# Kernel optimization log

Hardware: AMD Instinct MI355X
Metric: run time of the kernel (lower is better)

The kernel has to match this reference:

```python
import jax, jax.numpy as jnp
import numpy as np

B, T, F, U = 32, 2048, 512, 512


def hard_sigmoid(x):
    # Keras hard_sigmoid: clip(0.2*x + 0.5, 0, 1)
    return jnp.clip(0.2 * x + 0.5, 0.0, 1.0)


def setup_inputs() -> dict:
    key = jax.random.key(0)
    ks = jax.random.split(key, 10)
    s = 0.05  # keep pre-activations in a sane range
    return {
        "x": jax.random.normal(ks[0], (B, F), jnp.float32),
        "h": jax.random.normal(ks[1], (B, U), jnp.float32),
        "annotations": jax.random.normal(ks[2], (B, T, F), jnp.float32),
        "kernel": jax.random.normal(ks[3], (F, 3 * U), jnp.float32) * s,
        "recurrent_kernel": jax.random.normal(ks[4], (U, 3 * U), jnp.float32) * s,
        "attention_kernel": jax.random.normal(ks[5], (F, 3 * U), jnp.float32) * s,
        "Wa": jax.random.normal(ks[6], (U, U), jnp.float32) * s,
        "Ua": jax.random.normal(ks[7], (F, U), jnp.float32) * s,
        "Va": jax.random.normal(ks[8], (U,), jnp.float32) * s,
        "bias": jnp.zeros((3 * U,), jnp.float32),
        "attention_bias": jnp.zeros((3 * U,), jnp.float32),
        "Wa_bias": jnp.zeros((U,), jnp.float32),
        "Ua_bias": jnp.zeros((U,), jnp.float32),
    }


def reference(x, h, annotations, kernel, recurrent_kernel, attention_kernel,
              Wa, Ua, Va, bias, attention_bias, Wa_bias, Ua_bias):
    u = h.shape[-1]
    # --- Bahdanau additive attention ---
    # pre: [B, T, U] = Wa h_{t-1} (broadcast over T) + Ua a_j
    pre = (h @ Wa + Wa_bias)[:, None, :] + annotations @ Ua + Ua_bias
    scores = jnp.einsum('btu,u->bt', jnp.tanh(pre), Va)          # [B, T]
    alpha = jax.nn.softmax(scores, axis=-1)                      # [B, T]
    c = jnp.einsum('bt,btf->bf', alpha, annotations)             # context [B, F]

    # --- GRU gates (reset_after=False, implementation 1 math, batched) ---
    xm = x @ kernel + bias                                       # [B, 3U]
    am = c @ attention_kernel + attention_bias                   # [B, 3U]
    x_z, x_r, x_h = xm[:, :u], xm[:, u:2 * u], xm[:, 2 * u:]
    a_z, a_r, a_h = am[:, :u], am[:, u:2 * u], am[:, 2 * u:]
    h_z = h @ recurrent_kernel[:, :u]
    h_r = h @ recurrent_kernel[:, u:2 * u]

    z = hard_sigmoid(x_z + h_z + a_z)                            # update gate
    r = hard_sigmoid(x_r + h_r + a_r)                            # reset gate
    hh = jnp.tanh(x_h + (r * h) @ recurrent_kernel[:, 2 * u:] + a_h)
    h_new = z * h + (1.0 - z) * hh
    return h_new
```

## Files before the change

kernel.cpp:

```cpp
#include <hip/hip_runtime.h>
#include <hip/hip_bf16.h>
#include <math.h>

#define BB 32
#define TT 2048
#define FF 512
#define UU 512

typedef __attribute__((ext_vector_type(4))) float f32x4;
typedef __attribute__((ext_vector_type(4))) short bf16x4;
typedef __attribute__((ext_vector_type(8))) short bf16x8;

__device__ inline short f2bf(float f) {
  union { __hip_bfloat16 h; short s; } u;
  u.h = __float2bfloat16(f);
  return u.s;
}

__device__ inline float bf2f(unsigned short s) {
  return __uint_as_float(((unsigned)s) << 16);
}

__device__ inline float tanh_fast(float x) {
  float e = __expf(2.0f * x);
  return 1.0f - 2.0f * __builtin_amdgcn_rcpf(e + 1.0f);
}


__global__ __launch_bounds__(256) void k01(
    const float* __restrict__ Ua, short* __restrict__ Up,
    const float* __restrict__ h, const float* __restrict__ Wa,
    const float* __restrict__ Wa_bias, const float* __restrict__ Ua_bias,
    float* __restrict__ hw) {
  const int bid = blockIdx.x;
  const int tid = threadIdx.x;
  if (bid < 128) {
    const int cell = bid * 4 + (tid >> 6);
    const int n16 = cell >> 4;
    const int k32 = cell & 15;
    const int l = tid & 63;
    const int n = n16 * 16 + (l & 15);
    const int g = l >> 4;
    bf16x8 v;
#pragma unroll
    for (int i = 0; i < 8; ++i) {
      int k = k32 * 32 + (i < 4 ? g * 4 + i : 16 + g * 4 + (i - 4));
      v[i] = f2bf(Ua[k * UU + n]);
    }
    *reinterpret_cast<bf16x8*>(Up + ((size_t)cell * 64 + l) * 8) = v;
  } else {
    int idx = (bid - 128) * 256 + tid;
    int b = idx >> 9;
    int u = idx & 511;
    float acc = Wa_bias[u] + Ua_bias[u];
    const float* hrow = h + b * UU;
#pragma unroll 8
    for (int f = 0; f < FF; ++f) acc += hrow[f] * Wa[f * UU + u];
    hw[idx] = acc;
  }
}

__global__ __launch_bounds__(512, 2) void k2_flash(
    const float* __restrict__ ann, const short* __restrict__ Up,
    const float* __restrict__ Va, const float* __restrict__ hw,
    float* __restrict__ mbuf, float* __restrict__ lbuf,
    float* __restrict__ cpart) {
  __shared__ short Af[65536];
  __shared__ float red[8][128];
  __shared__ float e_all[128];
  __shared__ float sred[128];
  __shared__ float wtmp[4];
  __shared__ float ctxp[8][512];
  const int tile = blockIdx.x;
  const int b = blockIdx.y;
  const int t0 = tile * 128;
  const int tid = threadIdx.x;
  const int w = tid >> 6;
  const int l = tid & 63;
  const int lo = l & 15;
  const int g = l >> 4;

  const float* annb = ann + ((size_t)b * TT + t0) * FF;
  const float* srow = annb + (size_t)(w * 16 + lo) * FF + g * 4;
  short* const afw = &Af[((w * 16) * 64 + l) * 8];

  const short* upb[4];
  upb[0] = Up + ((size_t)((w * 4 + 0) * 16) * 64 + l) * 8;
  upb[1] = Up + ((size_t)((w * 4 + 1) * 16) * 64 + l) * 8;
  upb[2] = Up + ((size_t)((w * 4 + 2) * 16) * 64 + l) * 8;
  upb[3] = Up + ((size_t)((w * 4 + 3) * 16) * 64 + l) * 8;

  f32x4 acc[8][4];
#pragma unroll
  for (int mf = 0; mf < 8; ++mf)
#pragma unroll
    for (int nf = 0; nf < 4; ++nf) acc[mf][nf] = (f32x4)0.f;

  f32x4 stg[2][2];
  bf16x8 bb[2][4];

  stg[0][0] = *reinterpret_cast<const f32x4*>(srow + 0 * 32);
  stg[0][1] = *reinterpret_cast<const f32x4*>(srow + 0 * 32 + 16);
  stg[1][0] = *reinterpret_cast<const f32x4*>(srow + 1 * 32);
  stg[1][1] = *reinterpret_cast<const f32x4*>(srow + 1 * 32 + 16);
#pragma unroll
  for (int nf = 0; nf < 4; ++nf) {
    bb[0][nf] = *reinterpret_cast<const bf16x8*>(upb[nf]);
    bb[1][nf] = *reinterpret_cast<const bf16x8*>(upb[nf] + 512);
  }
  {
    bf16x8 o;
    o[0] = f2bf(stg[0][0].x); o[1] = f2bf(stg[0][0].y);
    o[2] = f2bf(stg[0][0].z); o[3] = f2bf(stg[0][0].w);
    o[4] = f2bf(stg[0][1].x); o[5] = f2bf(stg[0][1].y);
    o[6] = f2bf(stg[0][1].z); o[7] = f2bf(stg[0][1].w);
    *reinterpret_cast<bf16x8*>(afw + 0 * 512) = o;
  }
  __syncthreads();

#pragma unroll
  for (int s = 0; s < 16; ++s) {
    if (s < 14) {
      stg[s & 1][0] = *reinterpret_cast<const f32x4*>(srow + (s + 2) * 32);
      stg[s & 1][1] = *reinterpret_cast<const f32x4*>(srow + (s + 2) * 32 + 16);
    }
    bf16x8 aA[8];
#pragma unroll
    for (int mf = 0; mf < 8; ++mf)
      aA[mf] = *reinterpret_cast<const bf16x8*>(
          &Af[((mf * 16 + s) * 64 + l) * 8]);
    __builtin_amdgcn_s_setprio(1);
#pragma unroll
    for (int mf = 0; mf < 8; ++mf)
#pragma unroll
      for (int nf = 0; nf < 4; ++nf)
        acc[mf][nf] = __builtin_amdgcn_mfma_f32_16x16x32_bf16(
            aA[mf], bb[s & 1][nf], acc[mf][nf], 0, 0, 0);
    __builtin_amdgcn_s_setprio(0);
    if (s < 14) {
#pragma unroll
      for (int nf = 0; nf < 4; ++nf)
        bb[s & 1][nf] =
            *reinterpret_cast<const bf16x8*>(upb[nf] + (s + 2) * 512);
    }
    if (s < 15) {
      const f32x4 c0 = stg[(s + 1) & 1][0];
      const f32x4 c1 = stg[(s + 1) & 1][1];
      bf16x8 o;
      o[0] = f2bf(c0.x); o[1] = f2bf(c0.y); o[2] = f2bf(c0.z); o[3] = f2bf(c0.w);
      o[4] = f2bf(c1.x); o[5] = f2bf(c1.y); o[6] = f2bf(c1.z); o[7] = f2bf(c1.w);
      *reinterpret_cast<bf16x8*>(afw + (s + 1) * 512) = o;
      asm volatile("s_waitcnt lgkmcnt(0)" ::: "memory");
      __builtin_amdgcn_s_barrier();
    }
  }
  __syncthreads();

  const float* hwb = hw + b * UU;
  float part[8][4];
#pragma unroll
  for (int mf = 0; mf < 8; ++mf)
#pragma unroll
    for (int r = 0; r < 4; ++r) part[mf][r] = 0.f;
#pragma unroll
  for (int nf = 0; nf < 4; ++nf) {
    const int u = w * 64 + nf * 16 + lo;
    const float hv = hwb[u];
    const float vv = Va[u];
#pragma unroll
    for (int mf = 0; mf < 8; ++mf)
#pragma unroll
      for (int r = 0; r < 4; ++r)
        part[mf][r] += tanh_fast(acc[mf][nf][r] + hv) * vv;
  }
#pragma unroll
  for (int mf = 0; mf < 8; ++mf)
#pragma unroll
    for (int r = 0; r < 4; ++r) {
      float s = part[mf][r];
      s += __shfl_xor(s, 1);
      s += __shfl_xor(s, 2);
      s += __shfl_xor(s, 4);
      s += __shfl_xor(s, 8);
      part[mf][r] = s;
    }
  if (lo == 0) {
#pragma unroll
    for (int mf = 0; mf < 8; ++mf)
#pragma unroll
      for (int r = 0; r < 4; ++r)
        red[w][mf * 16 + g * 4 + r] = part[mf][r];
  }
  __syncthreads();

  if (tid < 128) {
    float s = red[0][tid] + red[1][tid] + red[2][tid] + red[3][tid] +
              red[4][tid] + red[5][tid] + red[6][tid] + red[7][tid];
    sred[tid] = s;
    float m = s;
#pragma unroll
    for (int off = 1; off < 64; off <<= 1) m = fmaxf(m, __shfl_xor(m, off));
    if ((tid & 63) == 0) wtmp[tid >> 6] = m;
  }
  __syncthreads();
  if (tid < 128) {
    float m = fmaxf(wtmp[0], wtmp[1]);
    float e = __expf(sred[tid] - m);
    e_all[tid] = e;
    float ls = e;
#pragma unroll
    for (int off = 1; off < 64; off <<= 1) ls += __shfl_xor(ls, off);
    if ((tid & 63) == 0) wtmp[2 + (tid >> 6)] = ls;
    if (tid == 0) mbuf[b * 16 + tile] = m;
  }
  __syncthreads();
  if (tid == 0) lbuf[b * 16 + tile] = wtmp[2] + wtmp[3];

  {
    const int fo = tid & 63;
    const int ts = tid >> 6;
    const int kk2 = fo >> 2;
    const int gg = fo & 3;
    float a8[8];
#pragma unroll
    for (int j = 0; j < 8; ++j) a8[j] = 0.f;
#pragma unroll
    for (int it = 0; it < 16; ++it) {
      const int tl = (it + fo) & 15;
      const int t = ts * 16 + tl;
      const int entry = (ts * 16 + kk2) * 64 + gg * 16 + tl;
      bf16x8 v = *reinterpret_cast<const bf16x8*>(&Af[entry * 8]);
      const float e = e_all[t];
#pragma unroll
      for (int j = 0; j < 8; ++j)
        a8[j] += e * bf2f((unsigned short)v[j]);
    }
#pragma unroll
    for (int j = 0; j < 8; ++j) ctxp[ts][fo * 8 + j] = a8[j];
  }
  __syncthreads();
  {
    float s = 0.f;
#pragma unroll
    for (int ts2 = 0; ts2 < 8; ++ts2) s += ctxp[ts2][tid];
    const int fo2 = tid >> 3;
    const int j2 = tid & 7;
    const int f = (fo2 >> 2) * 32 +
                  ((j2 < 4) ? (fo2 & 3) * 4 + j2 : 16 + (fo2 & 3) * 4 + (j2 - 4));
    cpart[(size_t)(b * 16 + tile) * 512 + f] = s;
  }
}

__global__ __launch_bounds__(512) void k5a_gates(
    const float* __restrict__ x, const float* __restrict__ mbuf,
    const float* __restrict__ lbuf, const float* __restrict__ cpart,
    const float* __restrict__ h, const float* __restrict__ kern,
    const float* __restrict__ ak, const float* __restrict__ rk,
    float* __restrict__ Gp) {
  __shared__ float wsx[64][64], wsa[64][64], wsr[64][64];
  __shared__ float xs[32][64], cs[32][64], hs[32][64];
  __shared__ float lsm[512], lsl[512], lwinv[512];
  const int n0 = blockIdx.x * 64;
  const int kg = blockIdx.y;
  const int kg0 = kg * 64;
  const bool has_r = (n0 < 1024);
  const int tid = threadIdx.x;
  const int n = tid & 63;
  const int b0 = (tid >> 6) * 4;
  const int wrow = tid >> 3, wcol = (tid & 7) * 8;
  const int orow = tid >> 4, ocol = (tid & 15) * 4;
  float acc[4] = {0.f, 0.f, 0.f, 0.f};

  lsm[tid] = mbuf[tid];
  lsl[tid] = lbuf[tid];

  {
    const size_t wb = (size_t)(kg0 + wrow) * 1536 + n0 + wcol;
    *reinterpret_cast<float4*>(&wsx[wrow][wcol])     = *reinterpret_cast<const float4*>(kern + wb);
    *reinterpret_cast<float4*>(&wsx[wrow][wcol + 4]) = *reinterpret_cast<const float4*>(kern + wb + 4);
    *reinterpret_cast<float4*>(&wsa[wrow][wcol])     = *reinterpret_cast<const float4*>(ak + wb);
    *reinterpret_cast<float4*>(&wsa[wrow][wcol + 4]) = *reinterpret_cast<const float4*>(ak + wb + 4);
    if (has_r) {
      *reinterpret_cast<float4*>(&wsr[wrow][wcol])     = *reinterpret_cast<const float4*>(rk + wb);
      *reinterpret_cast<float4*>(&wsr[wrow][wcol + 4]) = *reinterpret_cast<const float4*>(rk + wb + 4);
    }
    *reinterpret_cast<float4*>(&xs[orow][ocol]) =
        *reinterpret_cast<const float4*>(x + orow * FF + kg0 + ocol);
    *reinterpret_cast<float4*>(&hs[orow][ocol]) =
        *reinterpret_cast<const float4*>(h + orow * UU + kg0 + ocol);
  }
  __syncthreads();

  if (tid < 32) {
    float M = -1e30f;
#pragma unroll
    for (int i = 0; i < 16; ++i) M = fmaxf(M, lsm[tid * 16 + i]);
    float D = 0.f;
#pragma unroll
    for (int i = 0; i < 16; ++i)
      D += __expf(lsm[tid * 16 + i] - M) * lsl[tid * 16 + i];
    const float inv = 1.f / D;
#pragma unroll
    for (int i = 0; i < 16; ++i)
      lwinv[tid * 16 + i] = __expf(lsm[tid * 16 + i] - M) * inv;
  }
  __syncthreads();

  {
    float4 cv = {0.f, 0.f, 0.f, 0.f};
#pragma unroll
    for (int i = 0; i < 16; ++i) {
      const float wi = lwinv[orow * 16 + i];
      const float4 cp = *reinterpret_cast<const float4*>(
          &cpart[(size_t)(orow * 16 + i) * 512 + kg0 + ocol]);
      cv.x += wi * cp.x; cv.y += wi * cp.y;
      cv.z += wi * cp.z; cv.w += wi * cp.w;
    }
    *reinterpret_cast<float4*>(&cs[orow][ocol]) = cv;
  }
  __syncthreads();

  if (has_r) {
#pragma unroll 8
    for (int k = 0; k < 64; ++k) {
      const float wx = wsx[k][n], wa = wsa[k][n], wr = wsr[k][n];
#pragma unroll
      for (int j = 0; j < 4; ++j)
        acc[j] += xs[b0 + j][k] * wx + cs[b0 + j][k] * wa + hs[b0 + j][k] * wr;
    }
  } else {
#pragma unroll 8
    for (int k = 0; k < 64; ++k) {
      const float wx = wsx[k][n], wa = wsa[k][n];
#pragma unroll
      for (int j = 0; j < 4; ++j)
        acc[j] += xs[b0 + j][k] * wx + cs[b0 + j][k] * wa;
    }
  }
#pragma unroll
  for (int j = 0; j < 4; ++j)
    Gp[(size_t)kg * 49152 + (size_t)(b0 + j) * 1536 + n0 + n] = acc[j];
}

__global__ __launch_bounds__(512) void k5c_q(
    const float* __restrict__ Gp, const float* __restrict__ h,
    const float* __restrict__ bias, const float* __restrict__ abias,
    const float* __restrict__ rk, float* __restrict__ qp) {
  __shared__ float wsr[64][64];
  __shared__ float rs[32][64];
  const int n0 = blockIdx.x * 64;
  const int kg = blockIdx.y;
  const int kg0 = kg * 64;
  const int tid = threadIdx.x;
  const int n = tid & 63;
  const int b0 = (tid >> 6) * 4;
  const int wrow = tid >> 3, wcol = (tid & 7) * 8;
  const int orow = tid >> 4, ocol = (tid & 15) * 4;
  float acc[4] = {0.f, 0.f, 0.f, 0.f};

  {
    const size_t wb = (size_t)(kg0 + wrow) * 1536 + 1024 + n0 + wcol;
    *reinterpret_cast<float4*>(&wsr[wrow][wcol])     = *reinterpret_cast<const float4*>(rk + wb);
    *reinterpret_cast<float4*>(&wsr[wrow][wcol + 4]) = *reinterpret_cast<const float4*>(rk + wb + 4);
  }
  {
    const int u = kg0 + ocol;
    float4 sr = *reinterpret_cast<const float4*>(bias + 512 + u);
    const float4 ab = *reinterpret_cast<const float4*>(abias + 512 + u);
    sr.x += ab.x; sr.y += ab.y; sr.z += ab.z; sr.w += ab.w;
#pragma unroll
    for (int p = 0; p < 8; ++p) {
      const float4 gp4 = *reinterpret_cast<const float4*>(
          Gp + (size_t)p * 49152 + (size_t)orow * 1536 + 512 + u);
      sr.x += gp4.x; sr.y += gp4.y; sr.z += gp4.z; sr.w += gp4.w;
    }
    const float4 hv = *reinterpret_cast<const float4*>(h + orow * UU + u);
    rs[orow][ocol]     = fminf(fmaxf(0.2f * sr.x + 0.5f, 0.f), 1.f) * hv.x;
    rs[orow][ocol + 1] = fminf(fmaxf(0.2f * sr.y + 0.5f, 0.f), 1.f) * hv.y;
    rs[orow][ocol + 2] = fminf(fmaxf(0.2f * sr.z + 0.5f, 0.f), 1.f) * hv.z;
    rs[orow][ocol + 3] = fminf(fmaxf(0.2f * sr.w + 0.5f, 0.f), 1.f) * hv.w;
  }
  __syncthreads();
#pragma unroll 8
  for (int k = 0; k < 64; ++k) {
    const float w = wsr[k][n];
#pragma unroll
    for (int j = 0; j < 4; ++j) acc[j] += rs[b0 + j][k] * w;
  }
#pragma unroll
  for (int j = 0; j < 4; ++j)
    qp[(size_t)kg * 16384 + (b0 + j) * UU + n0 + n] = acc[j];
}

__global__ __launch_bounds__(256) void k5d_out(
    const float* __restrict__ Gp, const float* __restrict__ qp,
    const float* __restrict__ h, const float* __restrict__ bias,
    const float* __restrict__ abias, float* __restrict__ out) {
  int idx = blockIdx.x * blockDim.x + threadIdx.x;
  int b = idx >> 9;
  int u = idx & 511;
  float sz = bias[u] + abias[u];
  float sh = bias[1024 + u] + abias[1024 + u];
  const float* gb = Gp + (size_t)b * 1536;
  const float* qb = qp + (size_t)b * 512;
#pragma unroll
  for (int p = 0; p < 8; ++p) {
    sz += gb[(size_t)p * 49152 + u];
    sh += gb[(size_t)p * 49152 + 1024 + u] + qb[(size_t)p * 16384 + u];
  }
  float z = fminf(fmaxf(0.2f * sz + 0.5f, 0.f), 1.f);
  float hh = tanhf(sh);
  out[idx] = z * h[idx] + (1.f - z) * hh;
}

extern "C" void kernel_launch(void* const* d_in, const int* in_sizes, int n_in,
                              void* d_out, int out_size, void* d_ws, size_t ws_size,
                              hipStream_t stream) {
  const float* x       = (const float*)d_in[0];
  const float* h       = (const float*)d_in[1];
  const float* ann     = (const float*)d_in[2];
  const float* kern    = (const float*)d_in[3];
  const float* rk      = (const float*)d_in[4];
  const float* ak      = (const float*)d_in[5];
  const float* Wa      = (const float*)d_in[6];
  const float* Ua      = (const float*)d_in[7];
  const float* Va      = (const float*)d_in[8];
  const float* bias    = (const float*)d_in[9];
  const float* abias   = (const float*)d_in[10];
  const float* Wa_bias = (const float*)d_in[11];
  const float* Ua_bias = (const float*)d_in[12];

  float* ws     = (float*)d_ws;
  float* hw     = ws;
  float* mbuf   = ws + 16384;
  float* lbuf   = ws + 16896;
  float* cpart  = ws + 17408;
  float* Gp     = ws + 279552;
  float* qp     = ws + 672768;
  short* Up     = (short*)(ws + 803840);

  k01<<<192, 256, 0, stream>>>(Ua, Up, h, Wa, Wa_bias, Ua_bias, hw);

  dim3 g2(TT / 128, BB);
  k2_flash<<<g2, 512, 0, stream>>>(ann, Up, Va, hw, mbuf, lbuf, cpart);

  dim3 g5a(24, 8);
  k5a_gates<<<g5a, 512, 0, stream>>>(x, mbuf, lbuf, cpart, h, kern, ak, rk, Gp);

  dim3 g5c(8, 8);
  k5c_q<<<g5c, 512, 0, stream>>>(Gp, h, bias, abias, rk, qp);

  k5d_out<<<64, 256, 0, stream>>>(Gp, qp, h, bias, abias, (float*)d_out);
}
```

Baseline: 96.29 us.

## Halve attention tile to 64 timesteps to raise occupancy and CU coverage

```diff
diff --git a/kernel.cpp b/kernel.cpp
--- a/kernel.cpp
+++ b/kernel.cpp
@@ -60,29 +60,29 @@
   }
 }
 
-__global__ __launch_bounds__(512, 2) void k2_flash(
+__global__ __launch_bounds__(512, 4) void k2_flash(
     const float* __restrict__ ann, const short* __restrict__ Up,
     const float* __restrict__ Va, const float* __restrict__ hw,
     float* __restrict__ mbuf, float* __restrict__ lbuf,
     float* __restrict__ cpart) {
-  __shared__ short Af[65536];
-  __shared__ float red[8][128];
-  __shared__ float e_all[128];
-  __shared__ float sred[128];
-  __shared__ float wtmp[4];
-  __shared__ float ctxp[8][512];
+  __shared__ short Af[32768];
+  __shared__ float red[8][64];
+  __shared__ float e_all[64];
+  __shared__ float ctxp[4][512];
   const int tile = blockIdx.x;
   const int b = blockIdx.y;
-  const int t0 = tile * 128;
+  const int t0 = tile * 64;
   const int tid = threadIdx.x;
   const int w = tid >> 6;
   const int l = tid & 63;
   const int lo = l & 15;
   const int g = l >> 4;
+  const int mfs = w >> 1;
+  const int hh = w & 1;
 
   const float* annb = ann + ((size_t)b * TT + t0) * FF;
-  const float* srow = annb + (size_t)(w * 16 + lo) * FF + g * 4;
-  short* const afw = &Af[((w * 16) * 64 + l) * 8];
+  const float* srow = annb + (size_t)(mfs * 16 + lo) * FF + hh * 16 + g * 4;
+  short* const afw = &Af[mfs * 8192 + l * 8 + hh * 4];
 
   const short* upb[4];
   upb[0] = Up + ((size_t)((w * 4 + 0) * 16) * 64 + l) * 8;
@@ -90,52 +90,44 @@
   upb[2] = Up + ((size_t)((w * 4 + 2) * 16) * 64 + l) * 8;
   upb[3] = Up + ((size_t)((w * 4 + 3) * 16) * 64 + l) * 8;
 
-  f32x4 acc[8][4];
-#pragma unroll
-  for (int mf = 0; mf < 8; ++mf)
+  f32x4 acc[4][4];
+#pragma unroll
+  for (int mf = 0; mf < 4; ++mf)
 #pragma unroll
     for (int nf = 0; nf < 4; ++nf) acc[mf][nf] = (f32x4)0.f;
 
-  f32x4 stg[2][2];
+  f32x4 stg[2];
   bf16x8 bb[2][4];
 
-  stg[0][0] = *reinterpret_cast<const f32x4*>(srow + 0 * 32);
-  stg[0][1] = *reinterpret_cast<const f32x4*>(srow + 0 * 32 + 16);
-  stg[1][0] = *reinterpret_cast<const f32x4*>(srow + 1 * 32);
-  stg[1][1] = *reinterpret_cast<const f32x4*>(srow + 1 * 32 + 16);
+  stg[0] = *reinterpret_cast<const f32x4*>(srow + 0 * 32);
+  stg[1] = *reinterpret_cast<const f32x4*>(srow + 1 * 32);
 #pragma unroll
   for (int nf = 0; nf < 4; ++nf) {
     bb[0][nf] = *reinterpret_cast<const bf16x8*>(upb[nf]);
     bb[1][nf] = *reinterpret_cast<const bf16x8*>(upb[nf] + 512);
   }
   {
-    bf16x8 o;
-    o[0] = f2bf(stg[0][0].x); o[1] = f2bf(stg[0][0].y);
-    o[2] = f2bf(stg[0][0].z); o[3] = f2bf(stg[0][0].w);
-    o[4] = f2bf(stg[0][1].x); o[5] = f2bf(stg[0][1].y);
-    o[6] = f2bf(stg[0][1].z); o[7] = f2bf(stg[0][1].w);
-    *reinterpret_cast<bf16x8*>(afw + 0 * 512) = o;
+    bf16x4 o;
+    o[0] = f2bf(stg[0].x); o[1] = f2bf(stg[0].y);
+    o[2] = f2bf(stg[0].z); o[3] = f2bf(stg[0].w);
+    *reinterpret_cast<bf16x4*>(afw) = o;
   }
   __syncthreads();
 
 #pragma unroll
   for (int s = 0; s < 16; ++s) {
-    if (s < 14) {
-      stg[s & 1][0] = *reinterpret_cast<const f32x4*>(srow + (s + 2) * 32);
-      stg[s & 1][1] = *reinterpret_cast<const f32x4*>(srow + (s + 2) * 32 + 16);
-    }
-    bf16x8 aA[8];
-#pragma unroll
-    for (int mf = 0; mf < 8; ++mf)
-      aA[mf] = *reinterpret_cast<const bf16x8*>(
-          &Af[((mf * 16 + s) * 64 + l) * 8]);
+    if (s < 14)
+      stg[s & 1] = *reinterpret_cast<const f32x4*>(srow + (s + 2) * 32);
     __builtin_amdgcn_s_setprio(1);
 #pragma unroll
-    for (int mf = 0; mf < 8; ++mf)
+    for (int mf = 0; mf < 4; ++mf) {
+      bf16x8 a = *reinterpret_cast<const bf16x8*>(
+          &Af[mf * 8192 + s * 512 + l * 8]);
 #pragma unroll
       for (int nf = 0; nf < 4; ++nf)
         acc[mf][nf] = __builtin_amdgcn_mfma_f32_16x16x32_bf16(
-            aA[mf], bb[s & 1][nf], acc[mf][nf], 0, 0, 0);
+            a, bb[s & 1][nf], acc[mf][nf], 0, 0, 0);
+    }
     __builtin_amdgcn_s_setprio(0);
     if (s < 14) {
 #pragma unroll
@@ -144,12 +136,11 @@
             *reinterpret_cast<const bf16x8*>(upb[nf] + (s + 2) * 512);
     }
     if (s < 15) {
-      const f32x4 c0 = stg[(s + 1) & 1][0];
-      const f32x4 c1 = stg[(s + 1) & 1][1];
-      bf16x8 o;
-      o[0] = f2bf(c0.x); o[1] = f2bf(c0.y); o[2] = f2bf(c0.z); o[3] = f2bf(c0.w);
-      o[4] = f2bf(c1.x); o[5] = f2bf(c1.y); o[6] = f2bf(c1.z); o[7] = f2bf(c1.w);
-      *reinterpret_cast<bf16x8*>(afw + (s + 1) * 512) = o;
+      const f32x4 c0 = stg[(s + 1) & 1];
+      bf16x4 o;
+      o[0] = f2bf(c0.x); o[1] = f2bf(c0.y);
+      o[2] = f2bf(c0.z); o[3] = f2bf(c0.w);
+      *reinterpret_cast<bf16x4*>(afw + (s + 1) * 512) = o;
       asm volatile("s_waitcnt lgkmcnt(0)" ::: "memory");
       __builtin_amdgcn_s_barrier();
     }
@@ -157,9 +148,9 @@
   __syncthreads();
 
   const float* hwb = hw + b * UU;
-  float part[8][4];
-#pragma unroll
-  for (int mf = 0; mf < 8; ++mf)
+  float part[4][4];
+#pragma unroll
+  for (int mf = 0; mf < 4; ++mf)
 #pragma unroll
     for (int r = 0; r < 4; ++r) part[mf][r] = 0.f;
 #pragma unroll
@@ -168,13 +159,13 @@
     const float hv = hwb[u];
     const float vv = Va[u];
 #pragma unroll
-    for (int mf = 0; mf < 8; ++mf)
+    for (int mf = 0; mf < 4; ++mf)
 #pragma unroll
       for (int r = 0; r < 4; ++r)
         part[mf][r] += tanh_fast(acc[mf][nf][r] + hv) * vv;
   }
 #pragma unroll
-  for (int mf = 0; mf < 8; ++mf)
+  for (int mf = 0; mf < 4; ++mf)
 #pragma unroll
     for (int r = 0; r < 4; ++r) {
       float s = part[mf][r];
@@ -186,37 +177,32 @@
     }
   if (lo == 0) {
 #pragma unroll
-    for (int mf = 0; mf < 8; ++mf)
+    for (int mf = 0; mf < 4; ++mf)
 #pragma unroll
       for (int r = 0; r < 4; ++r)
         red[w][mf * 16 + g * 4 + r] = part[mf][r];
   }
   __syncthreads();
 
-  if (tid < 128) {
+  if (tid < 64) {
     float s = red[0][tid] + red[1][tid] + red[2][tid] + red[3][tid] +
               red[4][tid] + red[5][tid] + red[6][tid] + red[7][tid];
-    sred[tid] = s;
     float m = s;
 #pragma unroll
     for (int off = 1; off < 64; off <<= 1) m = fmaxf(m, __shfl_xor(m, off));
-    if ((tid & 63) == 0) wtmp[tid >> 6] = m;
-  }
-  __syncthreads();
-  if (tid < 128) {
-    float m = fmaxf(wtmp[0], wtmp[1]);
-    float e = __expf(sred[tid] - m);
+    float e = __expf(s - m);
     e_all[tid] = e;
     float ls = e;
 #pragma unroll
     for (int off = 1; off < 64; off <<= 1) ls += __shfl_xor(ls, off);
-    if ((tid & 63) == 0) wtmp[2 + (tid >> 6)] = ls;
-    if (tid == 0) mbuf[b * 16 + tile] = m;
-  }
-  __syncthreads();
-  if (tid == 0) lbuf[b * 16 + tile] = wtmp[2] + wtmp[3];
-
-  {
+    if (tid == 0) {
+      mbuf[b * 32 + tile] = m;
+      lbuf[b * 32 + tile] = ls;
+    }
+  }
+  __syncthreads();
+
+  if (tid < 256) {
     const int fo = tid & 63;
     const int ts = tid >> 6;
     const int kk2 = fo >> 2;
@@ -228,7 +214,7 @@
     for (int it = 0; it < 16; ++it) {
       const int tl = (it + fo) & 15;
       const int t = ts * 16 + tl;
-      const int entry = (ts * 16 + kk2) * 64 + gg * 16 + tl;
+      const int entry = ((t >> 4) * 16 + kk2) * 64 + gg * 16 + tl;
       bf16x8 v = *reinterpret_cast<const bf16x8*>(&Af[entry * 8]);
       const float e = e_all[t];
 #pragma unroll
@@ -240,14 +226,12 @@
   }
   __syncthreads();
   {
-    float s = 0.f;
-#pragma unroll
-    for (int ts2 = 0; ts2 < 8; ++ts2) s += ctxp[ts2][tid];
+    float s = ctxp[0][tid] + ctxp[1][tid] + ctxp[2][tid] + ctxp[3][tid];
     const int fo2 = tid >> 3;
     const int j2 = tid & 7;
     const int f = (fo2 >> 2) * 32 +
                   ((j2 < 4) ? (fo2 & 3) * 4 + j2 : 16 + (fo2 & 3) * 4 + (j2 - 4));
-    cpart[(size_t)(b * 16 + tile) * 512 + f] = s;
+    cpart[(size_t)(b * 32 + tile) * 512 + f] = s;
   }
 }
 
@@ -259,7 +243,7 @@
     float* __restrict__ Gp) {
   __shared__ float wsx[64][64], wsa[64][64], wsr[64][64];
   __shared__ float xs[32][64], cs[32][64], hs[32][64];
-  __shared__ float lsm[512], lsl[512], lwinv[512];
+  __shared__ float lsm[1024], lsl[1024], lwinv[1024];
   const int n0 = blockIdx.x * 64;
   const int kg = blockIdx.y;
   const int kg0 = kg * 64;
@@ -272,7 +256,9 @@
   float acc[4] = {0.f, 0.f, 0.f, 0.f};
 
   lsm[tid] = mbuf[tid];
+  lsm[tid + 512] = mbuf[tid + 512];
   lsl[tid] = lbuf[tid];
+  lsl[tid + 512] = lbuf[tid + 512];
 
   {
     const size_t wb = (size_t)(kg0 + wrow) * 1536 + n0 + wcol;
@@ -294,25 +280,25 @@
   if (tid < 32) {
     float M = -1e30f;
 #pragma unroll
-    for (int i = 0; i < 16; ++i) M = fmaxf(M, lsm[tid * 16 + i]);
+    for (int i = 0; i < 32; ++i) M = fmaxf(M, lsm[tid * 32 + i]);
     float D = 0.f;
 #pragma unroll
-    for (int i = 0; i < 16; ++i)
-      D += __expf(lsm[tid * 16 + i] - M) * lsl[tid * 16 + i];
+    for (int i = 0; i < 32; ++i)
+      D += __expf(lsm[tid * 32 + i] - M) * lsl[tid * 32 + i];
     const float inv = 1.f / D;
 #pragma unroll
-    for (int i = 0; i < 16; ++i)
-      lwinv[tid * 16 + i] = __expf(lsm[tid * 16 + i] - M) * inv;
+    for (int i = 0; i < 32; ++i)
+      lwinv[tid * 32 + i] = __expf(lsm[tid * 32 + i] - M) * inv;
   }
   __syncthreads();
 
   {
     float4 cv = {0.f, 0.f, 0.f, 0.f};
 #pragma unroll
-    for (int i = 0; i < 16; ++i) {
-      const float wi = lwinv[orow * 16 + i];
+    for (int i = 0; i < 32; ++i) {
+      const float wi = lwinv[orow * 32 + i];
       const float4 cp = *reinterpret_cast<const float4*>(
-          &cpart[(size_t)(orow * 16 + i) * 512 + kg0 + ocol]);
+          &cpart[(size_t)(orow * 32 + i) * 512 + kg0 + ocol]);
       cv.x += wi * cp.x; cv.y += wi * cp.y;
       cv.z += wi * cp.z; cv.w += wi * cp.w;
     }
@@ -433,15 +419,15 @@
   float* ws     = (float*)d_ws;
   float* hw     = ws;
   float* mbuf   = ws + 16384;
-  float* lbuf   = ws + 16896;
-  float* cpart  = ws + 17408;
-  float* Gp     = ws + 279552;
-  float* qp     = ws + 672768;
-  short* Up     = (short*)(ws + 803840);
+  float* lbuf   = ws + 17408;
+  float* cpart  = ws + 18432;
+  float* Gp     = ws + 542720;
+  float* qp     = ws + 935936;
+  short* Up     = (short*)(ws + 1067008);
 
   k01<<<192, 256, 0, stream>>>(Ua, Up, h, Wa, Wa_bias, Ua_bias, hw);
 
-  dim3 g2(TT / 128, BB);
+  dim3 g2(TT / 64, BB);
   k2_flash<<<g2, 512, 0, stream>>>(ann, Up, Va, hw, mbuf, lbuf, cpart);
 
   dim3 g5a(24, 8);
```

Measured after the change: 109.5 us. 13.8% more time.

## Deepen annotation prefetch and halve barriers in flash attention; split prep kernel

Applied to the files above, without the earlier changes.

```diff
diff --git a/kernel.cpp b/kernel.cpp
--- a/kernel.cpp
+++ b/kernel.cpp
@@ -27,37 +27,34 @@
 }
 
 
-__global__ __launch_bounds__(256) void k01(
-    const float* __restrict__ Ua, short* __restrict__ Up,
+__global__ __launch_bounds__(256) void k1_hw(
     const float* __restrict__ h, const float* __restrict__ Wa,
     const float* __restrict__ Wa_bias, const float* __restrict__ Ua_bias,
     float* __restrict__ hw) {
-  const int bid = blockIdx.x;
-  const int tid = threadIdx.x;
-  if (bid < 128) {
-    const int cell = bid * 4 + (tid >> 6);
-    const int n16 = cell >> 4;
-    const int k32 = cell & 15;
-    const int l = tid & 63;
-    const int n = n16 * 16 + (l & 15);
-    const int g = l >> 4;
-    bf16x8 v;
-#pragma unroll
-    for (int i = 0; i < 8; ++i) {
-      int k = k32 * 32 + (i < 4 ? g * 4 + i : 16 + g * 4 + (i - 4));
-      v[i] = f2bf(Ua[k * UU + n]);
-    }
-    *reinterpret_cast<bf16x8*>(Up + ((size_t)cell * 64 + l) * 8) = v;
-  } else {
-    int idx = (bid - 128) * 256 + tid;
-    int b = idx >> 9;
-    int u = idx & 511;
-    float acc = Wa_bias[u] + Ua_bias[u];
-    const float* hrow = h + b * UU;
+  int idx = blockIdx.x * blockDim.x + threadIdx.x;
+  int b = idx >> 9;
+  int u = idx & 511;
+  float acc = Wa_bias[u] + Ua_bias[u];
+  const float* hrow = h + b * UU;
 #pragma unroll 8
-    for (int f = 0; f < FF; ++f) acc += hrow[f] * Wa[f * UU + u];
-    hw[idx] = acc;
-  }
+  for (int f = 0; f < FF; ++f) acc += hrow[f] * Wa[f * UU + u];
+  hw[idx] = acc;
+}
+
+__global__ __launch_bounds__(64) void k0_pack(
+    const float* __restrict__ Ua, short* __restrict__ Up) {
+  const int n16 = blockIdx.x;
+  const int k32 = blockIdx.y;
+  const int l = threadIdx.x;
+  const int n = n16 * 16 + (l & 15);
+  const int g = l >> 4;
+  bf16x8 v;
+#pragma unroll
+  for (int i = 0; i < 8; ++i) {
+    int k = k32 * 32 + (i < 4 ? g * 4 + i : 16 + g * 4 + (i - 4));
+    v[i] = f2bf(Ua[k * UU + n]);
+  }
+  *reinterpret_cast<bf16x8*>(Up + ((size_t)(n16 * 16 + k32) * 64 + l) * 8) = v;
 }
 
 __global__ __launch_bounds__(512, 2) void k2_flash(
@@ -96,33 +93,37 @@
 #pragma unroll
     for (int nf = 0; nf < 4; ++nf) acc[mf][nf] = (f32x4)0.f;
 
-  f32x4 stg[2][2];
+  f32x4 stg[4][2];
   bf16x8 bb[2][4];
 
-  stg[0][0] = *reinterpret_cast<const f32x4*>(srow + 0 * 32);
-  stg[0][1] = *reinterpret_cast<const f32x4*>(srow + 0 * 32 + 16);
-  stg[1][0] = *reinterpret_cast<const f32x4*>(srow + 1 * 32);
-  stg[1][1] = *reinterpret_cast<const f32x4*>(srow + 1 * 32 + 16);
+#pragma unroll
+  for (int c = 0; c < 4; ++c) {
+    stg[c][0] = *reinterpret_cast<const f32x4*>(srow + c * 32);
+    stg[c][1] = *reinterpret_cast<const f32x4*>(srow + c * 32 + 16);
+  }
 #pragma unroll
   for (int nf = 0; nf < 4; ++nf) {
     bb[0][nf] = *reinterpret_cast<const bf16x8*>(upb[nf]);
     bb[1][nf] = *reinterpret_cast<const bf16x8*>(upb[nf] + 512);
   }
-  {
+#pragma unroll
+  for (int c = 0; c < 2; ++c) {
     bf16x8 o;
-    o[0] = f2bf(stg[0][0].x); o[1] = f2bf(stg[0][0].y);
-    o[2] = f2bf(stg[0][0].z); o[3] = f2bf(stg[0][0].w);
-    o[4] = f2bf(stg[0][1].x); o[5] = f2bf(stg[0][1].y);
-    o[6] = f2bf(stg[0][1].z); o[7] = f2bf(stg[0][1].w);
-    *reinterpret_cast<bf16x8*>(afw + 0 * 512) = o;
+    o[0] = f2bf(stg[c][0].x); o[1] = f2bf(stg[c][0].y);
+    o[2] = f2bf(stg[c][0].z); o[3] = f2bf(stg[c][0].w);
+    o[4] = f2bf(stg[c][1].x); o[5] = f2bf(stg[c][1].y);
+    o[6] = f2bf(stg[c][1].z); o[7] = f2bf(stg[c][1].w);
+    *reinterpret_cast<bf16x8*>(afw + c * 512) = o;
   }
   __syncthreads();
 
 #pragma unroll
   for (int s = 0; s < 16; ++s) {
-    if (s < 14) {
-      stg[s & 1][0] = *reinterpret_cast<const f32x4*>(srow + (s + 2) * 32);
-      stg[s & 1][1] = *reinterpret_cast<const f32x4*>(srow + (s + 2) * 32 + 16);
+    if ((s & 1) == 0 && s <= 10) {
+      stg[s & 3][0] = *reinterpret_cast<const f32x4*>(srow + (s + 4) * 32);
+      stg[s & 3][1] = *reinterpret_cast<const f32x4*>(srow + (s + 4) * 32 + 16);
+      stg[(s + 1) & 3][0] = *reinterpret_cast<const f32x4*>(srow + (s + 5) * 32);
+      stg[(s + 1) & 3][1] = *reinterpret_cast<const f32x4*>(srow + (s + 5) * 32 + 16);
     }
     bf16x8 aA[8];
 #pragma unroll
@@ -143,13 +144,16 @@
         bb[s & 1][nf] =
             *reinterpret_cast<const bf16x8*>(upb[nf] + (s + 2) * 512);
     }
-    if (s < 15) {
-      const f32x4 c0 = stg[(s + 1) & 1][0];
-      const f32x4 c1 = stg[(s + 1) & 1][1];
-      bf16x8 o;
-      o[0] = f2bf(c0.x); o[1] = f2bf(c0.y); o[2] = f2bf(c0.z); o[3] = f2bf(c0.w);
-      o[4] = f2bf(c1.x); o[5] = f2bf(c1.y); o[6] = f2bf(c1.z); o[7] = f2bf(c1.w);
-      *reinterpret_cast<bf16x8*>(afw + (s + 1) * 512) = o;
+    if ((s & 1) == 1 && s <= 13) {
+#pragma unroll
+      for (int d = 1; d <= 2; ++d) {
+        const f32x4 c0 = stg[(s + d) & 3][0];
+        const f32x4 c1 = stg[(s + d) & 3][1];
+        bf16x8 o;
+        o[0] = f2bf(c0.x); o[1] = f2bf(c0.y); o[2] = f2bf(c0.z); o[3] = f2bf(c0.w);
+        o[4] = f2bf(c1.x); o[5] = f2bf(c1.y); o[6] = f2bf(c1.z); o[7] = f2bf(c1.w);
+        *reinterpret_cast<bf16x8*>(afw + (s + d) * 512) = o;
+      }
       asm volatile("s_waitcnt lgkmcnt(0)" ::: "memory");
       __builtin_amdgcn_s_barrier();
     }
@@ -250,6 +254,7 @@
     cpart[(size_t)(b * 16 + tile) * 512 + f] = s;
   }
 }
+
 
 __global__ __launch_bounds__(512) void k5a_gates(
     const float* __restrict__ x, const float* __restrict__ mbuf,
@@ -439,7 +444,10 @@
   float* qp     = ws + 672768;
   short* Up     = (short*)(ws + 803840);
 
-  k01<<<192, 256, 0, stream>>>(Ua, Up, h, Wa, Wa_bias, Ua_bias, hw);
+  dim3 g0(32, 16);
+  k0_pack<<<g0, 64, 0, stream>>>(Ua, Up);
+
+  k1_hw<<<64, 256, 0, stream>>>(h, Wa, Wa_bias, Ua_bias, hw);
 
   dim3 g2(TT / 128, BB);
   k2_flash<<<g2, 512, 0, stream>>>(ann, Up, Va, hw, mbuf, lbuf, cpart);
```

Result: slower. 103.4 us (+7.4%).
